# Kernel optimization log

Hardware: AMD Instinct MI355X
Metric: run time of the kernel (lower is better)

Reference implementation:

```python
import jax, jax.numpy as jnp
import numpy as np

D_MODEL = 512
HEAD = 64

def setup_inputs() -> dict:
    key = jax.random.key(0)
    ks = jax.random.split(key, 7)
    s_in = 1.0 / np.sqrt(D_MODEL)
    x = jax.random.normal(ks[0], (4, 4096, D_MODEL), dtype=jnp.float32)
    Wk = jax.random.uniform(ks[1], (D_MODEL, HEAD), jnp.float32, -s_in, s_in)
    bk = jax.random.uniform(ks[2], (HEAD,), jnp.float32, -s_in, s_in)
    Wq = jax.random.uniform(ks[3], (D_MODEL, HEAD), jnp.float32, -s_in, s_in)
    bq = jax.random.uniform(ks[4], (HEAD,), jnp.float32, -s_in, s_in)
    Wv = jax.random.uniform(ks[5], (D_MODEL, HEAD), jnp.float32, -s_in, s_in)
    bv = jax.random.uniform(ks[6], (HEAD,), jnp.float32, -s_in, s_in)
    return {"x": x, "Wk": Wk, "bk": bk, "Wq": Wq, "bq": bq, "Wv": Wv, "bv": bv}

def reference(x, Wk, bk, Wq, bq, Wv, bv):
    B, T, C = x.shape
    k = x @ Wk + bk            # [B,T,H]
    q = x @ Wq + bq            # [B,T,H]
    v = x @ Wv + bv            # [B,T,H]
    scale = C ** (-0.5)
    # NOTE: original computes k @ q^T (keys index rows), softmax over query axis
    w = jnp.einsum('bkh,bqh->bkq', k, q) * scale  # [B,T,T]
    w = jax.nn.softmax(w, axis=-1)
    out = jnp.einsum('bkq,bqh->bkh', w, v)        # [B,T,H]
    return out
```

## Files before the change

### kernel.cpp

```cpp
#include <hip/hip_runtime.h>


#define DM 512
#define HD 64
#define TSEQ 4096
#define KSCALE (1.4426950408889634f * 0.04419417382415922f)

typedef __attribute__((ext_vector_type(8))) __bf16 bf16x8;
typedef __attribute__((ext_vector_type(4))) __bf16 bf16x4;
typedef __attribute__((ext_vector_type(2))) __bf16 bf16x2;
typedef __attribute__((ext_vector_type(4))) float f32x4;
typedef __attribute__((ext_vector_type(16))) float f32x16;
typedef __attribute__((ext_vector_type(4))) unsigned int uint4v;

__device__ __forceinline__ float fast_exp2(float x) {
#if __has_builtin(__builtin_amdgcn_exp2f)
    return __builtin_amdgcn_exp2f(x);
#else
    return exp2f(x);
#endif
}

__device__ __forceinline__ bf16x8 ld_bf16x8(const unsigned short* p) {
    return __builtin_bit_cast(bf16x8, *(const uint4v*)p);
}
__device__ __forceinline__ f32x4 mfma16(bf16x8 a, bf16x8 b, f32x4 c) {
    return __builtin_amdgcn_mfma_f32_16x16x32_bf16(a, b, c, 0, 0, 0);
}
__device__ __forceinline__ f32x16 mfma32(bf16x8 a, bf16x8 b, f32x16 c) {
    return __builtin_amdgcn_mfma_f32_32x32x16_bf16(a, b, c, 0, 0, 0);
}

typedef const __attribute__((address_space(1))) unsigned int* gas_t;
typedef __attribute__((address_space(3))) unsigned int* las_t;
__device__ __forceinline__ void async_cp16(const void* g, void* l) {
    __builtin_amdgcn_global_load_lds((gas_t)(unsigned long long)g,
                                     (las_t)(unsigned int)(unsigned long long)l,
                                     16, 0, 0);
}

__global__ __launch_bounds__(256) void prep_wt(const float* __restrict__ Wk,
                                               const float* __restrict__ Wq,
                                               const float* __restrict__ Wv,
                                               unsigned short* __restrict__ WT) {
    int e = blockIdx.x * 256 + threadIdx.x;
    int m = e >> 15;
    int idx = e & 32767;
    int h = idx >> 9;
    int cc = idx & 511;
    const float* W = (m == 0) ? Wk : ((m == 1) ? Wq : Wv);
    float v = W[cc * HD + h];
    if (m == 0) v *= KSCALE;
    ((__bf16*)WT)[m * 32768 + h * DM + cc] = (__bf16)v;
}

__global__ __launch_bounds__(512, 4) void proj(const float* __restrict__ x,
                                               const unsigned short* __restrict__ WT,
                                               const float* __restrict__ bk,
                                               const float* __restrict__ bq,
                                               const float* __restrict__ bv,
                                               unsigned short* __restrict__ Kw,
                                               unsigned short* __restrict__ Qw,
                                               unsigned short* __restrict__ VTw) {
    __shared__ alignas(16) float xs[16384];
    const int tid = threadIdx.x;
    const int wv = tid >> 6, lane = tid & 63;
    const int c = lane & 15, quad = lane >> 4;
    const int ng = wv & 3, rg = wv >> 2;
    const int bx = blockIdx.x;
    const int n0 = ng * 16;

#pragma unroll
    for (int r = 0; r < 8; ++r) {
        int cid = r * 512 + tid;
        int row = cid >> 7, pos = cid & 127;
        int g = (pos & ~7) | ((pos ^ row) & 7);
        async_cp16((const char*)x + (size_t)(bx * 32 + row) * 2048 + g * 16,
                   (char*)xs + r * 8192 + wv * 1024);
    }
    __builtin_amdgcn_s_waitcnt(0x0f70);
    __syncthreads();

    const int arow = rg * 16 + c;
    const unsigned short* wtb = WT + (n0 + c) * DM + quad * 8;
    f32x4 acc[3];
#pragma unroll
    for (int m = 0; m < 3; ++m) acc[m] = (f32x4){0.f, 0.f, 0.f, 0.f};

#pragma unroll
    for (int ks = 0; ks < 16; ++ks) {
        int p0 = ks * 8 + quad * 2;
        int sp0 = (p0 & ~7) | ((p0 ^ arow) & 7);
        int sp1 = ((p0 + 1) & ~7) | (((p0 + 1) ^ arow) & 7);
        f32x4 xa = *(const f32x4*)((const char*)xs + arow * 2048 + sp0 * 16);
        f32x4 xb = *(const f32x4*)((const char*)xs + arow * 2048 + sp1 * 16);
        bf16x8 af;
        af[0] = (__bf16)xa[0]; af[1] = (__bf16)xa[1]; af[2] = (__bf16)xa[2]; af[3] = (__bf16)xa[3];
        af[4] = (__bf16)xb[0]; af[5] = (__bf16)xb[1]; af[6] = (__bf16)xb[2]; af[7] = (__bf16)xb[3];
#pragma unroll
        for (int m = 0; m < 3; ++m) {
            bf16x8 bf = ld_bf16x8(wtb + m * 32768 + ks * 32);
            acc[m] = mfma16(af, bf, acc[m]);
        }
    }

    const int row0 = bx * 32 + rg * 16 + quad * 4;
#pragma unroll
    for (int m = 0; m < 3; ++m) {
        const float* bp = (m == 0) ? bk : ((m == 1) ? bq : bv);
        float bias = bp[n0 + c];
        if (m == 0) bias *= KSCALE;
        if (m < 2) {
            __bf16* dst = (__bf16*)((m == 0) ? Kw : Qw);
#pragma unroll
            for (int r = 0; r < 4; ++r)
                dst[(row0 + r) * HD + n0 + c] = (__bf16)(acc[m][r] + bias);
        } else {
            bf16x4 pk;
#pragma unroll
            for (int r = 0; r < 4; ++r) pk[r] = (__bf16)(acc[m][r] + bias);
            int b = bx >> 7;
            int pj = bx & 127;
            int jsub = rg * 16 + quad * 4;
            *(bf16x4*)(VTw + (((size_t)(b * 128 + pj)) * 64 + n0 + c) * 32 + jsub) = pk;
        }
    }
}

__global__ __launch_bounds__(512, 2) void attn(const unsigned short* __restrict__ Kw,
                                               const unsigned short* __restrict__ Qw,
                                               const unsigned short* __restrict__ VTw,
                                               float* __restrict__ Op,
                                               float* __restrict__ Lp) {
    __shared__ alignas(16) char smem[131072];

    const int tid = threadIdx.x;
    const int wv = tid >> 6, lane = tid & 63;
    const int l5 = lane >> 5, l31 = lane & 31;
    const int rg = wv >> 2, jc = wv & 3;
    const int bx = blockIdx.x;
    const int batch = bx >> 6, js = (bx >> 5) & 1, tile = bx & 31;
    const int rowbase = batch * TSEQ + tile * 128;

    bf16x8 kf[2][4];
#pragma unroll
    for (int it = 0; it < 2; ++it) {
        const unsigned short* kp = Kw + (size_t)(rowbase + rg * 64 + it * 32 + l31) * HD;
#pragma unroll
        for (int ks = 0; ks < 4; ++ks) kf[it][ks] = ld_bf16x8(kp + ks * 16 + l5 * 8);
    }

    int qoff[4];
#pragma unroll
    for (int ks = 0; ks < 4; ++ks)
        qoff[ks] = l31 * 128 + (((ks * 2 + l5) ^ (l31 & 7)) * 16);
    int voff[2][2];
#pragma unroll
    for (int ht = 0; ht < 2; ++ht)
#pragma unroll
        for (int k2 = 0; k2 < 2; ++k2)
            voff[ht][k2] = (ht * 32 + l31) * 64 + (((k2 * 2 + l5) ^ (l31 & 3)) * 16);

    int qgo[4], vgo[4];
#pragma unroll
    for (int r = 0; r < 4; ++r) {
        qgo[r] = (r * 8 + (lane >> 3)) * 128 + (((lane & 7) ^ (lane >> 3)) * 16);
        vgo[r] = (r * 16 + (lane >> 2)) * 64 + (((lane & 3) ^ ((lane >> 2) & 3)) * 16);
    }
    const char* qg = (const char*)Qw + ((size_t)(batch * TSEQ + js * 2048 + jc * 32)) * 128;
    const char* vg = (const char*)VTw + ((size_t)(batch * 128 + js * 64 + jc)) * 4096;
    char* wbase = smem + wv * 16384;

    f32x16 o00, o01, o10, o11;
#pragma unroll
    for (int r = 0; r < 16; ++r) { o00[r] = 0.f; o01[r] = 0.f; o10[r] = 0.f; o11[r] = 0.f; }
    float lac0 = 0.f, lac1 = 0.f;

#pragma unroll
    for (int r = 0; r < 4; ++r) async_cp16(qg + qgo[r], wbase + r * 1024);
#pragma unroll
    for (int r = 0; r < 4; ++r) async_cp16(vg + vgo[r], wbase + 4096 + r * 1024);

    for (int jt = 0; jt < 16; ++jt) {
        if (jt < 15) {
            char* nb = wbase + ((jt + 1) & 1) * 8192;
            const char* qn = qg + (size_t)(jt + 1) * 16384;
            const char* vn = vg + (size_t)(jt + 1) * 16384;
#pragma unroll
            for (int r = 0; r < 4; ++r) async_cp16(qn + qgo[r], nb + r * 1024);
#pragma unroll
            for (int r = 0; r < 4; ++r) async_cp16(vn + vgo[r], nb + 4096 + r * 1024);
            __builtin_amdgcn_s_waitcnt(0x0f78);
        } else {
            __builtin_amdgcn_s_waitcnt(0x0f70);
        }
        const char* cb = wbase + (jt & 1) * 8192;
        const unsigned short* QL = (const unsigned short*)cb;
        const unsigned short* VL = (const unsigned short*)(cb + 4096);

        f32x16 s0, s1;
#pragma unroll
        for (int r = 0; r < 16; ++r) { s0[r] = 0.f; s1[r] = 0.f; }
#pragma unroll
        for (int ks = 0; ks < 4; ++ks) {
            bf16x8 qa = ld_bf16x8((const unsigned short*)((const char*)QL + qoff[ks]));
            s0 = mfma32(qa, kf[0][ks], s0);
            s1 = mfma32(qa, kf[1][ks], s1);
        }

        unsigned int pk0[8], pk1[8];
#pragma unroll
        for (int m = 0; m < 8; ++m) {
            float a0 = fast_exp2(s0[2 * m]), a1 = fast_exp2(s0[2 * m + 1]);
            float b0 = fast_exp2(s1[2 * m]), b1 = fast_exp2(s1[2 * m + 1]);
            lac0 += a0 + a1;
            lac1 += b0 + b1;
            bf16x2 ta; ta[0] = (__bf16)a0; ta[1] = (__bf16)a1;
            bf16x2 tb; tb[0] = (__bf16)b0; tb[1] = (__bf16)b1;
            pk0[m] = __builtin_bit_cast(unsigned int, ta);
            pk1[m] = __builtin_bit_cast(unsigned int, tb);
        }

#pragma unroll
        for (int k2 = 0; k2 < 2; ++k2) {
            bf16x8 pb0, pb1;
            {
                unsigned int A0 = pk0[k2 * 4 + 0], A1 = pk0[k2 * 4 + 1];
                unsigned int B0 = pk0[k2 * 4 + 2], B1 = pk0[k2 * 4 + 3];
                unsigned int t0 = l5 ? A0 : B0, t1 = l5 ? A1 : B1;
                unsigned int r0 = (unsigned int)__shfl_xor((int)t0, 32, 64);
                unsigned int r1 = (unsigned int)__shfl_xor((int)t1, 32, 64);
                uint4v u;
                u[0] = l5 ? r0 : A0; u[1] = l5 ? r1 : A1;
                u[2] = l5 ? B0 : r0; u[3] = l5 ? B1 : r1;
                pb0 = __builtin_bit_cast(bf16x8, u);
            }
            {
                unsigned int A0 = pk1[k2 * 4 + 0], A1 = pk1[k2 * 4 + 1];
                unsigned int B0 = pk1[k2 * 4 + 2], B1 = pk1[k2 * 4 + 3];
                unsigned int t0 = l5 ? A0 : B0, t1 = l5 ? A1 : B1;
                unsigned int r0 = (unsigned int)__shfl_xor((int)t0, 32, 64);
                unsigned int r1 = (unsigned int)__shfl_xor((int)t1, 32, 64);
                uint4v u;
                u[0] = l5 ? r0 : A0; u[1] = l5 ? r1 : A1;
                u[2] = l5 ? B0 : r0; u[3] = l5 ? B1 : r1;
                pb1 = __builtin_bit_cast(bf16x8, u);
            }
            bf16x8 vf0 = ld_bf16x8((const unsigned short*)((const char*)VL + voff[0][k2]));
            bf16x8 vf1 = ld_bf16x8((const unsigned short*)((const char*)VL + voff[1][k2]));
            o00 = mfma32(vf0, pb0, o00);
            o01 = mfma32(vf0, pb1, o01);
            o10 = mfma32(vf1, pb0, o10);
            o11 = mfma32(vf1, pb1, o11);
        }
    }

    lac0 += __shfl_xor(lac0, 32, 64);
    lac1 += __shfl_xor(lac1, 32, 64);
    __syncthreads();
    float* OCp = (float*)smem;
    float* ldsl = (float*)(smem + 34816);
    if (l5 == 0) {
        ldsl[jc * 128 + rg * 64 + l31] = lac0;
        ldsl[jc * 128 + rg * 64 + 32 + l31] = lac1;
    }

#pragma unroll
    for (int ph = 0; ph < 4; ++ph) {
        const int ht = ph >> 1, ih = ph & 1;
        __syncthreads();
        if (rg == ih) {
            const f32x16 oa = ht ? o10 : o00;
            const f32x16 ob = ht ? o11 : o01;
#pragma unroll
            for (int r = 0; r < 16; ++r) {
                int hr = (r & 3) + 8 * (r >> 2) + 4 * l5;
                OCp[(jc * 32 + hr) * 68 + l31] = oa[r];
                OCp[(jc * 32 + hr) * 68 + 32 + l31] = ob[r];
            }
        }
        __syncthreads();
#pragma unroll
        for (int rep = 0; rep < 4; ++rep) {
            int idx = rep * 512 + tid;
            int i = idx >> 5, hr = idx & 31;
            float v = OCp[(0 * 32 + hr) * 68 + i] + OCp[(1 * 32 + hr) * 68 + i]
                    + OCp[(2 * 32 + hr) * 68 + i] + OCp[(3 * 32 + hr) * 68 + i];
            Op[(size_t)js * 1048576 + (size_t)(rowbase + ih * 64 + i) * HD + ht * 32 + hr] = v;
        }
        if (ph == 0 && tid < 128) {
            float L = ldsl[tid] + ldsl[128 + tid] + ldsl[256 + tid] + ldsl[384 + tid];
            Lp[js * 16384 + rowbase + tid] = L;
        }
    }
}

__global__ __launch_bounds__(512) void fin(const float* __restrict__ Op,
                                           const float* __restrict__ Lp,
                                           float* __restrict__ out) {
    int idx = blockIdx.x * 512 + threadIdx.x;
    int e = idx * 4;
    int row = e >> 6;
    f32x4 a = *(const f32x4*)(Op + e);
    f32x4 b = *(const f32x4*)(Op + 1048576 + e);
    float L = Lp[row] + Lp[16384 + row];
    f32x4 r;
#pragma unroll
    for (int k = 0; k < 4; ++k) r[k] = (a[k] + b[k]) / L;
    *(f32x4*)(out + e) = r;
}

extern "C" void kernel_launch(void* const* d_in, const int* in_sizes, int n_in,
                              void* d_out, int out_size, void* d_ws, size_t ws_size,
                              hipStream_t stream) {
    (void)in_sizes; (void)n_in; (void)out_size; (void)ws_size;
    const float* x  = (const float*)d_in[0];
    const float* Wk = (const float*)d_in[1];
    const float* bk = (const float*)d_in[2];
    const float* Wq = (const float*)d_in[3];
    const float* bq = (const float*)d_in[4];
    const float* Wv = (const float*)d_in[5];
    const float* bv = (const float*)d_in[6];

    char* ws = (char*)d_ws;
    unsigned short* WT  = (unsigned short*)(ws);
    unsigned short* Kw  = (unsigned short*)(ws + 196608);
    unsigned short* Qw  = (unsigned short*)(ws + 2293760);
    unsigned short* VTw = (unsigned short*)(ws + 4390912);
    float* Opart        = (float*)(ws + 6488064);
    float* Lpart        = (float*)(ws + 14876672);
    float* outp = (float*)d_out;

    hipLaunchKernelGGL(prep_wt, dim3(384), dim3(256), 0, stream, Wk, Wq, Wv, WT);
    hipLaunchKernelGGL(proj, dim3(512), dim3(512), 0, stream,
                       x, WT, bk, bq, bv, Kw, Qw, VTw);
    hipLaunchKernelGGL(attn, dim3(256), dim3(512), 0, stream, Kw, Qw, VTw, Opart, Lpart);
    hipLaunchKernelGGL(fin, dim3(512), dim3(512), 0, stream, Opart, Lpart, outp);
}
```

Before: 138.9 us.

## Fuse all four stages into one cooperative kernel with grid syncs

```diff
diff --git a/kernel.cpp b/kernel.cpp
--- a/kernel.cpp
+++ b/kernel.cpp
@@ -1,10 +1,13 @@
 #include <hip/hip_runtime.h>
+#include <hip/hip_cooperative_groups.h>
 
 
 #define DM 512
 #define HD 64
 #define TSEQ 4096
 #define KSCALE (1.4426950408889634f * 0.04419417382415922f)
+
+namespace cg = cooperative_groups;
 
 typedef __attribute__((ext_vector_type(8))) __bf16 bf16x8;
 typedef __attribute__((ext_vector_type(4))) __bf16 bf16x4;
@@ -39,275 +42,290 @@
                                      16, 0, 0);
 }
 
-__global__ __launch_bounds__(256) void prep_wt(const float* __restrict__ Wk,
-                                               const float* __restrict__ Wq,
-                                               const float* __restrict__ Wv,
-                                               unsigned short* __restrict__ WT) {
-    int e = blockIdx.x * 256 + threadIdx.x;
-    int m = e >> 15;
-    int idx = e & 32767;
-    int h = idx >> 9;
-    int cc = idx & 511;
-    const float* W = (m == 0) ? Wk : ((m == 1) ? Wq : Wv);
-    float v = W[cc * HD + h];
-    if (m == 0) v *= KSCALE;
-    ((__bf16*)WT)[m * 32768 + h * DM + cc] = (__bf16)v;
-}
-
-__global__ __launch_bounds__(512, 4) void proj(const float* __restrict__ x,
-                                               const unsigned short* __restrict__ WT,
-                                               const float* __restrict__ bk,
-                                               const float* __restrict__ bq,
-                                               const float* __restrict__ bv,
-                                               unsigned short* __restrict__ Kw,
-                                               unsigned short* __restrict__ Qw,
-                                               unsigned short* __restrict__ VTw) {
-    __shared__ alignas(16) float xs[16384];
+__global__ __launch_bounds__(512) void mega(const float* __restrict__ x,
+                                            const float* __restrict__ Wk,
+                                            const float* __restrict__ bk,
+                                            const float* __restrict__ Wq,
+                                            const float* __restrict__ bq,
+                                            const float* __restrict__ Wv,
+                                            const float* __restrict__ bv,
+                                            unsigned short* __restrict__ WT,
+                                            unsigned short* __restrict__ Kw,
+                                            unsigned short* __restrict__ Qw,
+                                            unsigned short* __restrict__ VTw,
+                                            float* __restrict__ Op,
+                                            float* __restrict__ Lp,
+                                            float* __restrict__ out) {
+    __shared__ alignas(16) char smem[131072];
+    cg::grid_group grid = cg::this_grid();
+
     const int tid = threadIdx.x;
-    const int wv = tid >> 6, lane = tid & 63;
-    const int c = lane & 15, quad = lane >> 4;
-    const int ng = wv & 3, rg = wv >> 2;
-    const int bx = blockIdx.x;
-    const int n0 = ng * 16;
-
-#pragma unroll
-    for (int r = 0; r < 8; ++r) {
-        int cid = r * 512 + tid;
-        int row = cid >> 7, pos = cid & 127;
-        int g = (pos & ~7) | ((pos ^ row) & 7);
-        async_cp16((const char*)x + (size_t)(bx * 32 + row) * 2048 + g * 16,
-                   (char*)xs + r * 8192 + wv * 1024);
+    const int bxk = blockIdx.x;
+
+    if (tid < 384) {
+        int e = bxk * 384 + tid;
+        int m = e >> 15;
+        int idx = e & 32767;
+        int h = idx >> 9;
+        int cc = idx & 511;
+        const float* W = (m == 0) ? Wk : ((m == 1) ? Wq : Wv);
+        float v = W[cc * HD + h];
+        if (m == 0) v *= KSCALE;
+        ((__bf16*)WT)[m * 32768 + h * DM + cc] = (__bf16)v;
     }
-    __builtin_amdgcn_s_waitcnt(0x0f70);
-    __syncthreads();
-
-    const int arow = rg * 16 + c;
-    const unsigned short* wtb = WT + (n0 + c) * DM + quad * 8;
-    f32x4 acc[3];
-#pragma unroll
-    for (int m = 0; m < 3; ++m) acc[m] = (f32x4){0.f, 0.f, 0.f, 0.f};
-
-#pragma unroll
-    for (int ks = 0; ks < 16; ++ks) {
-        int p0 = ks * 8 + quad * 2;
-        int sp0 = (p0 & ~7) | ((p0 ^ arow) & 7);
-        int sp1 = ((p0 + 1) & ~7) | (((p0 + 1) ^ arow) & 7);
-        f32x4 xa = *(const f32x4*)((const char*)xs + arow * 2048 + sp0 * 16);
-        f32x4 xb = *(const f32x4*)((const char*)xs + arow * 2048 + sp1 * 16);
-        bf16x8 af;
-        af[0] = (__bf16)xa[0]; af[1] = (__bf16)xa[1]; af[2] = (__bf16)xa[2]; af[3] = (__bf16)xa[3];
-        af[4] = (__bf16)xb[0]; af[5] = (__bf16)xb[1]; af[6] = (__bf16)xb[2]; af[7] = (__bf16)xb[3];
-#pragma unroll
-        for (int m = 0; m < 3; ++m) {
-            bf16x8 bf = ld_bf16x8(wtb + m * 32768 + ks * 32);
-            acc[m] = mfma16(af, bf, acc[m]);
+    grid.sync();
+
+    {
+        const int wv = tid >> 6, lane = tid & 63;
+        const int c = lane & 15, quad = lane >> 4;
+        const int ng = wv & 3, rg = wv >> 2;
+        const int n0 = ng * 16;
+        const int arow = rg * 16 + c;
+
+#pragma unroll
+        for (int t = 0; t < 2; ++t) {
+            int bx = bxk * 2 + t;
+            float* xs = (float*)(smem + t * 65536);
+#pragma unroll
+            for (int r = 0; r < 8; ++r) {
+                int cid = r * 512 + tid;
+                int row = cid >> 7, pos = cid & 127;
+                int g = (pos & ~7) | ((pos ^ row) & 7);
+                async_cp16((const char*)x + (size_t)(bx * 32 + row) * 2048 + g * 16,
+                           (char*)xs + r * 8192 + wv * 1024);
+            }
+        }
+
+#pragma unroll
+        for (int t = 0; t < 2; ++t) {
+            int bx = bxk * 2 + t;
+            const float* xs = (const float*)(smem + t * 65536);
+            if (t == 0) __builtin_amdgcn_s_waitcnt(0x0f78);
+            else        __builtin_amdgcn_s_waitcnt(0x0f70);
+            __syncthreads();
+
+            const unsigned short* wtb = WT + (n0 + c) * DM + quad * 8;
+            f32x4 acc[3];
+#pragma unroll
+            for (int m = 0; m < 3; ++m) acc[m] = (f32x4){0.f, 0.f, 0.f, 0.f};
+
+#pragma unroll
+            for (int ks = 0; ks < 16; ++ks) {
+                int p0 = ks * 8 + quad * 2;
+                int sp0 = (p0 & ~7) | ((p0 ^ arow) & 7);
+                int sp1 = ((p0 + 1) & ~7) | (((p0 + 1) ^ arow) & 7);
+                f32x4 xa = *(const f32x4*)((const char*)xs + arow * 2048 + sp0 * 16);
+                f32x4 xb = *(const f32x4*)((const char*)xs + arow * 2048 + sp1 * 16);
+                bf16x8 af;
+                af[0] = (__bf16)xa[0]; af[1] = (__bf16)xa[1]; af[2] = (__bf16)xa[2]; af[3] = (__bf16)xa[3];
+                af[4] = (__bf16)xb[0]; af[5] = (__bf16)xb[1]; af[6] = (__bf16)xb[2]; af[7] = (__bf16)xb[3];
+#pragma unroll
+                for (int m = 0; m < 3; ++m) {
+                    bf16x8 bf = ld_bf16x8(wtb + m * 32768 + ks * 32);
+                    acc[m] = mfma16(af, bf, acc[m]);
+                }
+            }
+
+            const int row0 = bx * 32 + rg * 16 + quad * 4;
+#pragma unroll
+            for (int m = 0; m < 3; ++m) {
+                const float* bp = (m == 0) ? bk : ((m == 1) ? bq : bv);
+                float bias = bp[n0 + c];
+                if (m == 0) bias *= KSCALE;
+                if (m < 2) {
+                    __bf16* dst = (__bf16*)((m == 0) ? Kw : Qw);
+#pragma unroll
+                    for (int r = 0; r < 4; ++r)
+                        dst[(row0 + r) * HD + n0 + c] = (__bf16)(acc[m][r] + bias);
+                } else {
+                    bf16x4 pk;
+#pragma unroll
+                    for (int r = 0; r < 4; ++r) pk[r] = (__bf16)(acc[m][r] + bias);
+                    int b = bx >> 7;
+                    int pj = bx & 127;
+                    int jsub = rg * 16 + quad * 4;
+                    *(bf16x4*)(VTw + (((size_t)(b * 128 + pj)) * 64 + n0 + c) * 32 + jsub) = pk;
+                }
+            }
         }
     }
-
-    const int row0 = bx * 32 + rg * 16 + quad * 4;
-#pragma unroll
-    for (int m = 0; m < 3; ++m) {
-        const float* bp = (m == 0) ? bk : ((m == 1) ? bq : bv);
-        float bias = bp[n0 + c];
-        if (m == 0) bias *= KSCALE;
-        if (m < 2) {
-            __bf16* dst = (__bf16*)((m == 0) ? Kw : Qw);
-#pragma unroll
-            for (int r = 0; r < 4; ++r)
-                dst[(row0 + r) * HD + n0 + c] = (__bf16)(acc[m][r] + bias);
-        } else {
-            bf16x4 pk;
-#pragma unroll
-            for (int r = 0; r < 4; ++r) pk[r] = (__bf16)(acc[m][r] + bias);
-            int b = bx >> 7;
-            int pj = bx & 127;
-            int jsub = rg * 16 + quad * 4;
-            *(bf16x4*)(VTw + (((size_t)(b * 128 + pj)) * 64 + n0 + c) * 32 + jsub) = pk;
+    grid.sync();
+
+    {
+        const int wv = tid >> 6, lane = tid & 63;
+        const int l5 = lane >> 5, l31 = lane & 31;
+        const int rg = wv >> 2, jc = wv & 3;
+        const int bx = bxk;
+        const int batch = bx >> 6, js = (bx >> 5) & 1, tile = bx & 31;
+        const int rowbase = batch * TSEQ + tile * 128;
+
+        bf16x8 kf[2][4];
+#pragma unroll
+        for (int it = 0; it < 2; ++it) {
+            const unsigned short* kp = Kw + (size_t)(rowbase + rg * 64 + it * 32 + l31) * HD;
+#pragma unroll
+            for (int ks = 0; ks < 4; ++ks) kf[it][ks] = ld_bf16x8(kp + ks * 16 + l5 * 8);
+        }
+
+        int qoff[4];
+#pragma unroll
+        for (int ks = 0; ks < 4; ++ks)
+            qoff[ks] = l31 * 128 + (((ks * 2 + l5) ^ (l31 & 7)) * 16);
+        int voff[2][2];
+#pragma unroll
+        for (int ht = 0; ht < 2; ++ht)
+#pragma unroll
+            for (int k2 = 0; k2 < 2; ++k2)
+                voff[ht][k2] = (ht * 32 + l31) * 64 + (((k2 * 2 + l5) ^ (l31 & 3)) * 16);
+
+        int qgo[4], vgo[4];
+#pragma unroll
+        for (int r = 0; r < 4; ++r) {
+            qgo[r] = (r * 8 + (lane >> 3)) * 128 + (((lane & 7) ^ (lane >> 3)) * 16);
+            vgo[r] = (r * 16 + (lane >> 2)) * 64 + (((lane & 3) ^ ((lane >> 2) & 3)) * 16);
+        }
+        const char* qg = (const char*)Qw + ((size_t)(batch * TSEQ + js * 2048 + jc * 32)) * 128;
+        const char* vg = (const char*)VTw + ((size_t)(batch * 128 + js * 64 + jc)) * 4096;
+        char* wbase = smem + wv * 16384;
+
+        f32x16 o00, o01, o10, o11;
+#pragma unroll
+        for (int r = 0; r < 16; ++r) { o00[r] = 0.f; o01[r] = 0.f; o10[r] = 0.f; o11[r] = 0.f; }
+        float lac0 = 0.f, lac1 = 0.f;
+
+#pragma unroll
+        for (int r = 0; r < 4; ++r) async_cp16(qg + qgo[r], wbase + r * 1024);
+#pragma unroll
+        for (int r = 0; r < 4; ++r) async_cp16(vg + vgo[r], wbase + 4096 + r * 1024);
+
+        for (int jt = 0; jt < 16; ++jt) {
+            if (jt < 15) {
+                char* nb = wbase + ((jt + 1) & 1) * 8192;
+                const char* qn = qg + (size_t)(jt + 1) * 16384;
+                const char* vn = vg + (size_t)(jt + 1) * 16384;
+#pragma unroll
+                for (int r = 0; r < 4; ++r) async_cp16(qn + qgo[r], nb + r * 1024);
+#pragma unroll
+                for (int r = 0; r < 4; ++r) async_cp16(vn + vgo[r], nb + 4096 + r * 1024);
+                __builtin_amdgcn_s_waitcnt(0x0f78);
+            } else {
+                __builtin_amdgcn_s_waitcnt(0x0f70);
+            }
+            const char* cb = wbase + (jt & 1) * 8192;
+            const unsigned short* QL = (const unsigned short*)cb;
+            const unsigned short* VL = (const unsigned short*)(cb + 4096);
+
+            f32x16 s0, s1;
+#pragma unroll
+            for (int r = 0; r < 16; ++r) { s0[r] = 0.f; s1[r] = 0.f; }
+#pragma unroll
+            for (int ks = 0; ks < 4; ++ks) {
+                bf16x8 qa = ld_bf16x8((const unsigned short*)((const char*)QL + qoff[ks]));
+                s0 = mfma32(qa, kf[0][ks], s0);
+                s1 = mfma32(qa, kf[1][ks], s1);
+            }
+
+            unsigned int pk0[8], pk1[8];
+#pragma unroll
+            for (int m = 0; m < 8; ++m) {
+                float a0 = fast_exp2(s0[2 * m]), a1 = fast_exp2(s0[2 * m + 1]);
+                float b0 = fast_exp2(s1[2 * m]), b1 = fast_exp2(s1[2 * m + 1]);
+                lac0 += a0 + a1;
+                lac1 += b0 + b1;
+                bf16x2 ta; ta[0] = (__bf16)a0; ta[1] = (__bf16)a1;
+                bf16x2 tb; tb[0] = (__bf16)b0; tb[1] = (__bf16)b1;
+                pk0[m] = __builtin_bit_cast(unsigned int, ta);
+                pk1[m] = __builtin_bit_cast(unsigned int, tb);
+            }
+
+#pragma unroll
+            for (int k2 = 0; k2 < 2; ++k2) {
+                bf16x8 pb0, pb1;
+                {
+                    unsigned int A0 = pk0[k2 * 4 + 0], A1 = pk0[k2 * 4 + 1];
+                    unsigned int B0 = pk0[k2 * 4 + 2], B1 = pk0[k2 * 4 + 3];
+                    unsigned int t0 = l5 ? A0 : B0, t1 = l5 ? A1 : B1;
+                    unsigned int r0 = (unsigned int)__shfl_xor((int)t0, 32, 64);
+                    unsigned int r1 = (unsigned int)__shfl_xor((int)t1, 32, 64);
+                    uint4v u;
+                    u[0] = l5 ? r0 : A0; u[1] = l5 ? r1 : A1;
+                    u[2] = l5 ? B0 : r0; u[3] = l5 ? B1 : r1;
+                    pb0 = __builtin_bit_cast(bf16x8, u);
+                }
+                {
+                    unsigned int A0 = pk1[k2 * 4 + 0], A1 = pk1[k2 * 4 + 1];
+                    unsigned int B0 = pk1[k2 * 4 + 2], B1 = pk1[k2 * 4 + 3];
+                    unsigned int t0 = l5 ? A0 : B0, t1 = l5 ? A1 : B1;
+                    unsigned int r0 = (unsigned int)__shfl_xor((int)t0, 32, 64);
+                    unsigned int r1 = (unsigned int)__shfl_xor((int)t1, 32, 64);
+                    uint4v u;
+                    u[0] = l5 ? r0 : A0; u[1] = l5 ? r1 : A1;
+                    u[2] = l5 ? B0 : r0; u[3] = l5 ? B1 : r1;
+                    pb1 = __builtin_bit_cast(bf16x8, u);
+                }
+                bf16x8 vf0 = ld_bf16x8((const unsigned short*)((const char*)VL + voff[0][k2]));
+                bf16x8 vf1 = ld_bf16x8((const unsigned short*)((const char*)VL + voff[1][k2]));
+                o00 = mfma32(vf0, pb0, o00);
+                o01 = mfma32(vf0, pb1, o01);
+                o10 = mfma32(vf1, pb0, o10);
+                o11 = mfma32(vf1, pb1, o11);
+            }
+        }
+
+        lac0 += __shfl_xor(lac0, 32, 64);
+        lac1 += __shfl_xor(lac1, 32, 64);
+        __syncthreads();
+        float* OCp = (float*)smem;
+        float* ldsl = (float*)(smem + 34816);
+        if (l5 == 0) {
+            ldsl[jc * 128 + rg * 64 + l31] = lac0;
+            ldsl[jc * 128 + rg * 64 + 32 + l31] = lac1;
+        }
+
+#pragma unroll
+        for (int ph = 0; ph < 4; ++ph) {
+            const int ht = ph >> 1, ih = ph & 1;
+            __syncthreads();
+            if (rg == ih) {
+                const f32x16 oa = ht ? o10 : o00;
+                const f32x16 ob = ht ? o11 : o01;
+#pragma unroll
+                for (int r = 0; r < 16; ++r) {
+                    int hr = (r & 3) + 8 * (r >> 2) + 4 * l5;
+                    OCp[(jc * 32 + hr) * 68 + l31] = oa[r];
+                    OCp[(jc * 32 + hr) * 68 + 32 + l31] = ob[r];
+                }
+            }
+            __syncthreads();
+#pragma unroll
+            for (int rep = 0; rep < 4; ++rep) {
+                int idx = rep * 512 + tid;
+                int i = idx >> 5, hr = idx & 31;
+                float v = OCp[(0 * 32 + hr) * 68 + i] + OCp[(1 * 32 + hr) * 68 + i]
+                        + OCp[(2 * 32 + hr) * 68 + i] + OCp[(3 * 32 + hr) * 68 + i];
+                Op[(size_t)js * 1048576 + (size_t)(rowbase + ih * 64 + i) * HD + ht * 32 + hr] = v;
+            }
+            if (ph == 0 && tid < 128) {
+                float L = ldsl[tid] + ldsl[128 + tid] + ldsl[256 + tid] + ldsl[384 + tid];
+                Lp[js * 16384 + rowbase + tid] = L;
+            }
         }
     }
-}
-
-__global__ __launch_bounds__(512, 2) void attn(const unsigned short* __restrict__ Kw,
-                                               const unsigned short* __restrict__ Qw,
-                                               const unsigned short* __restrict__ VTw,
-                                               float* __restrict__ Op,
-                                               float* __restrict__ Lp) {
-    __shared__ alignas(16) char smem[131072];
-
-    const int tid = threadIdx.x;
-    const int wv = tid >> 6, lane = tid & 63;
-    const int l5 = lane >> 5, l31 = lane & 31;
-    const int rg = wv >> 2, jc = wv & 3;
-    const int bx = blockIdx.x;
-    const int batch = bx >> 6, js = (bx >> 5) & 1, tile = bx & 31;
-    const int rowbase = batch * TSEQ + tile * 128;
-
-    bf16x8 kf[2][4];
-#pragma unroll
-    for (int it = 0; it < 2; ++it) {
-        const unsigned short* kp = Kw + (size_t)(rowbase + rg * 64 + it * 32 + l31) * HD;
-#pragma unroll
-        for (int ks = 0; ks < 4; ++ks) kf[it][ks] = ld_bf16x8(kp + ks * 16 + l5 * 8);
+    grid.sync();
+
+#pragma unroll
+    for (int t = 0; t < 2; ++t) {
+        int idx = bxk * 1024 + t * 512 + tid;
+        int e = idx * 4;
+        int row = e >> 6;
+        f32x4 a = *(const f32x4*)(Op + e);
+        f32x4 b = *(const f32x4*)(Op + 1048576 + e);
+        float L = Lp[row] + Lp[16384 + row];
+        f32x4 r;
+#pragma unroll
+        for (int k = 0; k < 4; ++k) r[k] = (a[k] + b[k]) / L;
+        *(f32x4*)(out + e) = r;
     }
-
-    int qoff[4];
-#pragma unroll
-    for (int ks = 0; ks < 4; ++ks)
-        qoff[ks] = l31 * 128 + (((ks * 2 + l5) ^ (l31 & 7)) * 16);
-    int voff[2][2];
-#pragma unroll
-    for (int ht = 0; ht < 2; ++ht)
-#pragma unroll
-        for (int k2 = 0; k2 < 2; ++k2)
-            voff[ht][k2] = (ht * 32 + l31) * 64 + (((k2 * 2 + l5) ^ (l31 & 3)) * 16);
-
-    int qgo[4], vgo[4];
-#pragma unroll
-    for (int r = 0; r < 4; ++r) {
-        qgo[r] = (r * 8 + (lane >> 3)) * 128 + (((lane & 7) ^ (lane >> 3)) * 16);
-        vgo[r] = (r * 16 + (lane >> 2)) * 64 + (((lane & 3) ^ ((lane >> 2) & 3)) * 16);
-    }
-    const char* qg = (const char*)Qw + ((size_t)(batch * TSEQ + js * 2048 + jc * 32)) * 128;
-    const char* vg = (const char*)VTw + ((size_t)(batch * 128 + js * 64 + jc)) * 4096;
-    char* wbase = smem + wv * 16384;
-
-    f32x16 o00, o01, o10, o11;
-#pragma unroll
-    for (int r = 0; r < 16; ++r) { o00[r] = 0.f; o01[r] = 0.f; o10[r] = 0.f; o11[r] = 0.f; }
-    float lac0 = 0.f, lac1 = 0.f;
-
-#pragma unroll
-    for (int r = 0; r < 4; ++r) async_cp16(qg + qgo[r], wbase + r * 1024);
-#pragma unroll
-    for (int r = 0; r < 4; ++r) async_cp16(vg + vgo[r], wbase + 4096 + r * 1024);
-
-    for (int jt = 0; jt < 16; ++jt) {
-        if (jt < 15) {
-            char* nb = wbase + ((jt + 1) & 1) * 8192;
-            const char* qn = qg + (size_t)(jt + 1) * 16384;
-            const char* vn = vg + (size_t)(jt + 1) * 16384;
-#pragma unroll
-            for (int r = 0; r < 4; ++r) async_cp16(qn + qgo[r], nb + r * 1024);
-#pragma unroll
-            for (int r = 0; r < 4; ++r) async_cp16(vn + vgo[r], nb + 4096 + r * 1024);
-            __builtin_amdgcn_s_waitcnt(0x0f78);
-        } else {
-            __builtin_amdgcn_s_waitcnt(0x0f70);
-        }
-        const char* cb = wbase + (jt & 1) * 8192;
-        const unsigned short* QL = (const unsigned short*)cb;
-        const unsigned short* VL = (const unsigned short*)(cb + 4096);
-
-        f32x16 s0, s1;
-#pragma unroll
-        for (int r = 0; r < 16; ++r) { s0[r] = 0.f; s1[r] = 0.f; }
-#pragma unroll
-        for (int ks = 0; ks < 4; ++ks) {
-            bf16x8 qa = ld_bf16x8((const unsigned short*)((const char*)QL + qoff[ks]));
-            s0 = mfma32(qa, kf[0][ks], s0);
-            s1 = mfma32(qa, kf[1][ks], s1);
-        }
-
-        unsigned int pk0[8], pk1[8];
-#pragma unroll
-        for (int m = 0; m < 8; ++m) {
-            float a0 = fast_exp2(s0[2 * m]), a1 = fast_exp2(s0[2 * m + 1]);
-            float b0 = fast_exp2(s1[2 * m]), b1 = fast_exp2(s1[2 * m + 1]);
-            lac0 += a0 + a1;
-            lac1 += b0 + b1;
-            bf16x2 ta; ta[0] = (__bf16)a0; ta[1] = (__bf16)a1;
-            bf16x2 tb; tb[0] = (__bf16)b0; tb[1] = (__bf16)b1;
-            pk0[m] = __builtin_bit_cast(unsigned int, ta);
-            pk1[m] = __builtin_bit_cast(unsigned int, tb);
-        }
-
-#pragma unroll
-        for (int k2 = 0; k2 < 2; ++k2) {
-            bf16x8 pb0, pb1;
-            {
-                unsigned int A0 = pk0[k2 * 4 + 0], A1 = pk0[k2 * 4 + 1];
-                unsigned int B0 = pk0[k2 * 4 + 2], B1 = pk0[k2 * 4 + 3];
-                unsigned int t0 = l5 ? A0 : B0, t1 = l5 ? A1 : B1;
-                unsigned int r0 = (unsigned int)__shfl_xor((int)t0, 32, 64);
-                unsigned int r1 = (unsigned int)__shfl_xor((int)t1, 32, 64);
-                uint4v u;
-                u[0] = l5 ? r0 : A0; u[1] = l5 ? r1 : A1;
-                u[2] = l5 ? B0 : r0; u[3] = l5 ? B1 : r1;
-                pb0 = __builtin_bit_cast(bf16x8, u);
-            }
-            {
-                unsigned int A0 = pk1[k2 * 4 + 0], A1 = pk1[k2 * 4 + 1];
-                unsigned int B0 = pk1[k2 * 4 + 2], B1 = pk1[k2 * 4 + 3];
-                unsigned int t0 = l5 ? A0 : B0, t1 = l5 ? A1 : B1;
-                unsigned int r0 = (unsigned int)__shfl_xor((int)t0, 32, 64);
-                unsigned int r1 = (unsigned int)__shfl_xor((int)t1, 32, 64);
-                uint4v u;
-                u[0] = l5 ? r0 : A0; u[1] = l5 ? r1 : A1;
-                u[2] = l5 ? B0 : r0; u[3] = l5 ? B1 : r1;
-                pb1 = __builtin_bit_cast(bf16x8, u);
-            }
-            bf16x8 vf0 = ld_bf16x8((const unsigned short*)((const char*)VL + voff[0][k2]));
-            bf16x8 vf1 = ld_bf16x8((const unsigned short*)((const char*)VL + voff[1][k2]));
-            o00 = mfma32(vf0, pb0, o00);
-            o01 = mfma32(vf0, pb1, o01);
-            o10 = mfma32(vf1, pb0, o10);
-            o11 = mfma32(vf1, pb1, o11);
-        }
-    }
-
-    lac0 += __shfl_xor(lac0, 32, 64);
-    lac1 += __shfl_xor(lac1, 32, 64);
-    __syncthreads();
-    float* OCp = (float*)smem;
-    float* ldsl = (float*)(smem + 34816);
-    if (l5 == 0) {
-        ldsl[jc * 128 + rg * 64 + l31] = lac0;
-        ldsl[jc * 128 + rg * 64 + 32 + l31] = lac1;
-    }
-
-#pragma unroll
-    for (int ph = 0; ph < 4; ++ph) {
-        const int ht = ph >> 1, ih = ph & 1;
-        __syncthreads();
-        if (rg == ih) {
-            const f32x16 oa = ht ? o10 : o00;
-            const f32x16 ob = ht ? o11 : o01;
-#pragma unroll
-            for (int r = 0; r < 16; ++r) {
-                int hr = (r & 3) + 8 * (r >> 2) + 4 * l5;
-                OCp[(jc * 32 + hr) * 68 + l31] = oa[r];
-                OCp[(jc * 32 + hr) * 68 + 32 + l31] = ob[r];
-            }
-        }
-        __syncthreads();
-#pragma unroll
-        for (int rep = 0; rep < 4; ++rep) {
-            int idx = rep * 512 + tid;
-            int i = idx >> 5, hr = idx & 31;
-            float v = OCp[(0 * 32 + hr) * 68 + i] + OCp[(1 * 32 + hr) * 68 + i]
-                    + OCp[(2 * 32 + hr) * 68 + i] + OCp[(3 * 32 + hr) * 68 + i];
-            Op[(size_t)js * 1048576 + (size_t)(rowbase + ih * 64 + i) * HD + ht * 32 + hr] = v;
-        }
-        if (ph == 0 && tid < 128) {
-            float L = ldsl[tid] + ldsl[128 + tid] + ldsl[256 + tid] + ldsl[384 + tid];
-            Lp[js * 16384 + rowbase + tid] = L;
-        }
-    }
-}
-
-__global__ __launch_bounds__(512) void fin(const float* __restrict__ Op,
-                                           const float* __restrict__ Lp,
-                                           float* __restrict__ out) {
-    int idx = blockIdx.x * 512 + threadIdx.x;
-    int e = idx * 4;
-    int row = e >> 6;
-    f32x4 a = *(const f32x4*)(Op + e);
-    f32x4 b = *(const f32x4*)(Op + 1048576 + e);
-    float L = Lp[row] + Lp[16384 + row];
-    f32x4 r;
-#pragma unroll
-    for (int k = 0; k < 4; ++k) r[k] = (a[k] + b[k]) / L;
-    *(f32x4*)(out + e) = r;
 }
 
 extern "C" void kernel_launch(void* const* d_in, const int* in_sizes, int n_in,
@@ -331,9 +349,8 @@
     float* Lpart        = (float*)(ws + 14876672);
     float* outp = (float*)d_out;
 
-    hipLaunchKernelGGL(prep_wt, dim3(384), dim3(256), 0, stream, Wk, Wq, Wv, WT);
-    hipLaunchKernelGGL(proj, dim3(512), dim3(512), 0, stream,
-                       x, WT, bk, bq, bv, Kw, Qw, VTw);
-    hipLaunchKernelGGL(attn, dim3(256), dim3(512), 0, stream, Kw, Qw, VTw, Opart, Lpart);
-    hipLaunchKernelGGL(fin, dim3(512), dim3(512), 0, stream, Opart, Lpart, outp);
-}
+    void* args[] = {(void*)&x, (void*)&Wk, (void*)&bk, (void*)&Wq, (void*)&bq,
+                    (void*)&Wv, (void*)&bv, (void*)&WT, (void*)&Kw, (void*)&Qw,
+                    (void*)&VTw, (void*)&Opart, (void*)&Lpart, (void*)&outp};
+    hipLaunchCooperativeKernel((void*)mega, dim3(256), dim3(512), args, 0, stream);
+}
```

Measured after the change: 234.6 us. 68.9% more time.

## Load attention Q/V fragments directly into registers and halve proj tile size

Applied to the files above, without the earlier changes.

```diff
diff --git a/kernel.cpp b/kernel.cpp
--- a/kernel.cpp
+++ b/kernel.cpp
@@ -54,7 +54,7 @@
     ((__bf16*)WT)[m * 32768 + h * DM + cc] = (__bf16)v;
 }
 
-__global__ __launch_bounds__(512, 4) void proj(const float* __restrict__ x,
+__global__ __launch_bounds__(256, 4) void proj(const float* __restrict__ x,
                                                const unsigned short* __restrict__ WT,
                                                const float* __restrict__ bk,
                                                const float* __restrict__ bq,
@@ -62,26 +62,24 @@
                                                unsigned short* __restrict__ Kw,
                                                unsigned short* __restrict__ Qw,
                                                unsigned short* __restrict__ VTw) {
-    __shared__ alignas(16) float xs[16384];
+    __shared__ alignas(16) float xs[8192];
     const int tid = threadIdx.x;
     const int wv = tid >> 6, lane = tid & 63;
     const int c = lane & 15, quad = lane >> 4;
-    const int ng = wv & 3, rg = wv >> 2;
     const int bx = blockIdx.x;
-    const int n0 = ng * 16;
+    const int n0 = wv * 16;
 
 #pragma unroll
     for (int r = 0; r < 8; ++r) {
-        int cid = r * 512 + tid;
+        int cid = r * 256 + tid;
         int row = cid >> 7, pos = cid & 127;
         int g = (pos & ~7) | ((pos ^ row) & 7);
-        async_cp16((const char*)x + (size_t)(bx * 32 + row) * 2048 + g * 16,
-                   (char*)xs + r * 8192 + wv * 1024);
+        async_cp16((const char*)x + (size_t)(bx * 16 + row) * 2048 + g * 16,
+                   (char*)xs + r * 4096 + wv * 1024);
     }
     __builtin_amdgcn_s_waitcnt(0x0f70);
     __syncthreads();
 
-    const int arow = rg * 16 + c;
     const unsigned short* wtb = WT + (n0 + c) * DM + quad * 8;
     f32x4 acc[3];
 #pragma unroll
@@ -90,10 +88,10 @@
 #pragma unroll
     for (int ks = 0; ks < 16; ++ks) {
         int p0 = ks * 8 + quad * 2;
-        int sp0 = (p0 & ~7) | ((p0 ^ arow) & 7);
-        int sp1 = ((p0 + 1) & ~7) | (((p0 + 1) ^ arow) & 7);
-        f32x4 xa = *(const f32x4*)((const char*)xs + arow * 2048 + sp0 * 16);
-        f32x4 xb = *(const f32x4*)((const char*)xs + arow * 2048 + sp1 * 16);
+        int sp0 = (p0 & ~7) | ((p0 ^ c) & 7);
+        int sp1 = ((p0 + 1) & ~7) | (((p0 + 1) ^ c) & 7);
+        f32x4 xa = *(const f32x4*)((const char*)xs + c * 2048 + sp0 * 16);
+        f32x4 xb = *(const f32x4*)((const char*)xs + c * 2048 + sp1 * 16);
         bf16x8 af;
         af[0] = (__bf16)xa[0]; af[1] = (__bf16)xa[1]; af[2] = (__bf16)xa[2]; af[3] = (__bf16)xa[3];
         af[4] = (__bf16)xb[0]; af[5] = (__bf16)xb[1]; af[6] = (__bf16)xb[2]; af[7] = (__bf16)xb[3];
@@ -104,7 +102,7 @@
         }
     }
 
-    const int row0 = bx * 32 + rg * 16 + quad * 4;
+    const int row0 = bx * 16 + quad * 4;
 #pragma unroll
     for (int m = 0; m < 3; ++m) {
         const float* bp = (m == 0) ? bk : ((m == 1) ? bq : bv);
@@ -119,9 +117,10 @@
             bf16x4 pk;
 #pragma unroll
             for (int r = 0; r < 4; ++r) pk[r] = (__bf16)(acc[m][r] + bias);
-            int b = bx >> 7;
-            int pj = bx & 127;
-            int jsub = rg * 16 + quad * 4;
+            int b = bx >> 8;
+            int t16 = bx & 255;
+            int pj = t16 >> 1;
+            int jsub = (t16 & 1) * 16 + quad * 4;
             *(bf16x4*)(VTw + (((size_t)(b * 128 + pj)) * 64 + n0 + c) * 32 + jsub) = pk;
         }
     }
@@ -132,7 +131,7 @@
                                                const unsigned short* __restrict__ VTw,
                                                float* __restrict__ Op,
                                                float* __restrict__ Lp) {
-    __shared__ alignas(16) char smem[131072];
+    __shared__ alignas(16) char smem[36864];
 
     const int tid = threadIdx.x;
     const int wv = tid >> 6, lane = tid & 63;
@@ -150,62 +149,48 @@
         for (int ks = 0; ks < 4; ++ks) kf[it][ks] = ld_bf16x8(kp + ks * 16 + l5 * 8);
     }
 
-    int qoff[4];
-#pragma unroll
-    for (int ks = 0; ks < 4; ++ks)
-        qoff[ks] = l31 * 128 + (((ks * 2 + l5) ^ (l31 & 7)) * 16);
-    int voff[2][2];
-#pragma unroll
-    for (int ht = 0; ht < 2; ++ht)
-#pragma unroll
-        for (int k2 = 0; k2 < 2; ++k2)
-            voff[ht][k2] = (ht * 32 + l31) * 64 + (((k2 * 2 + l5) ^ (l31 & 3)) * 16);
-
-    int qgo[4], vgo[4];
-#pragma unroll
-    for (int r = 0; r < 4; ++r) {
-        qgo[r] = (r * 8 + (lane >> 3)) * 128 + (((lane & 7) ^ (lane >> 3)) * 16);
-        vgo[r] = (r * 16 + (lane >> 2)) * 64 + (((lane & 3) ^ ((lane >> 2) & 3)) * 16);
-    }
-    const char* qg = (const char*)Qw + ((size_t)(batch * TSEQ + js * 2048 + jc * 32)) * 128;
-    const char* vg = (const char*)VTw + ((size_t)(batch * 128 + js * 64 + jc)) * 4096;
-    char* wbase = smem + wv * 16384;
+    const char* qg = (const char*)Qw
+                   + ((size_t)(batch * TSEQ + js * 2048 + jc * 32 + l31)) * 128
+                   + l5 * 16;
+    const char* vg = (const char*)VTw
+                   + ((size_t)(batch * 128 + js * 64 + jc)) * 4096
+                   + l31 * 64 + l5 * 16;
 
     f32x16 o00, o01, o10, o11;
 #pragma unroll
     for (int r = 0; r < 16; ++r) { o00[r] = 0.f; o01[r] = 0.f; o10[r] = 0.f; o11[r] = 0.f; }
     float lac0 = 0.f, lac1 = 0.f;
 
-#pragma unroll
-    for (int r = 0; r < 4; ++r) async_cp16(qg + qgo[r], wbase + r * 1024);
-#pragma unroll
-    for (int r = 0; r < 4; ++r) async_cp16(vg + vgo[r], wbase + 4096 + r * 1024);
+    bf16x8 qa[4], vf[2][2];
+#pragma unroll
+    for (int ks = 0; ks < 4; ++ks) qa[ks] = ld_bf16x8((const unsigned short*)(qg + ks * 32));
+#pragma unroll
+    for (int ht = 0; ht < 2; ++ht)
+#pragma unroll
+        for (int k2 = 0; k2 < 2; ++k2)
+            vf[ht][k2] = ld_bf16x8((const unsigned short*)(vg + ht * 2048 + k2 * 32));
 
     for (int jt = 0; jt < 16; ++jt) {
+        bf16x8 qn[4], vn[2][2];
         if (jt < 15) {
-            char* nb = wbase + ((jt + 1) & 1) * 8192;
-            const char* qn = qg + (size_t)(jt + 1) * 16384;
-            const char* vn = vg + (size_t)(jt + 1) * 16384;
-#pragma unroll
-            for (int r = 0; r < 4; ++r) async_cp16(qn + qgo[r], nb + r * 1024);
-#pragma unroll
-            for (int r = 0; r < 4; ++r) async_cp16(vn + vgo[r], nb + 4096 + r * 1024);
-            __builtin_amdgcn_s_waitcnt(0x0f78);
-        } else {
-            __builtin_amdgcn_s_waitcnt(0x0f70);
-        }
-        const char* cb = wbase + (jt & 1) * 8192;
-        const unsigned short* QL = (const unsigned short*)cb;
-        const unsigned short* VL = (const unsigned short*)(cb + 4096);
+            const char* q1 = qg + (size_t)(jt + 1) * 16384;
+            const char* v1 = vg + (size_t)(jt + 1) * 16384;
+#pragma unroll
+            for (int ks = 0; ks < 4; ++ks) qn[ks] = ld_bf16x8((const unsigned short*)(q1 + ks * 32));
+#pragma unroll
+            for (int ht = 0; ht < 2; ++ht)
+#pragma unroll
+                for (int k2 = 0; k2 < 2; ++k2)
+                    vn[ht][k2] = ld_bf16x8((const unsigned short*)(v1 + ht * 2048 + k2 * 32));
+        }
 
         f32x16 s0, s1;
 #pragma unroll
         for (int r = 0; r < 16; ++r) { s0[r] = 0.f; s1[r] = 0.f; }
 #pragma unroll
         for (int ks = 0; ks < 4; ++ks) {
-            bf16x8 qa = ld_bf16x8((const unsigned short*)((const char*)QL + qoff[ks]));
-            s0 = mfma32(qa, kf[0][ks], s0);
-            s1 = mfma32(qa, kf[1][ks], s1);
+            s0 = mfma32(qa[ks], kf[0][ks], s0);
+            s1 = mfma32(qa[ks], kf[1][ks], s1);
         }
 
         unsigned int pk0[8], pk1[8];
@@ -246,13 +231,18 @@
                 u[2] = l5 ? B0 : r0; u[3] = l5 ? B1 : r1;
                 pb1 = __builtin_bit_cast(bf16x8, u);
             }
-            bf16x8 vf0 = ld_bf16x8((const unsigned short*)((const char*)VL + voff[0][k2]));
-            bf16x8 vf1 = ld_bf16x8((const unsigned short*)((const char*)VL + voff[1][k2]));
-            o00 = mfma32(vf0, pb0, o00);
-            o01 = mfma32(vf0, pb1, o01);
-            o10 = mfma32(vf1, pb0, o10);
-            o11 = mfma32(vf1, pb1, o11);
-        }
+            o00 = mfma32(vf[0][k2], pb0, o00);
+            o01 = mfma32(vf[0][k2], pb1, o01);
+            o10 = mfma32(vf[1][k2], pb0, o10);
+            o11 = mfma32(vf[1][k2], pb1, o11);
+        }
+
+#pragma unroll
+        for (int ks = 0; ks < 4; ++ks) qa[ks] = qn[ks];
+#pragma unroll
+        for (int ht = 0; ht < 2; ++ht)
+#pragma unroll
+            for (int k2 = 0; k2 < 2; ++k2) vf[ht][k2] = vn[ht][k2];
     }
 
     lac0 += __shfl_xor(lac0, 32, 64);
@@ -332,7 +322,7 @@
     float* outp = (float*)d_out;
 
     hipLaunchKernelGGL(prep_wt, dim3(384), dim3(256), 0, stream, Wk, Wq, Wv, WT);
-    hipLaunchKernelGGL(proj, dim3(512), dim3(512), 0, stream,
+    hipLaunchKernelGGL(proj, dim3(1024), dim3(256), 0, stream,
                        x, WT, bk, bq, bv, Kw, Qw, VTw);
     hipLaunchKernelGGL(attn, dim3(256), dim3(512), 0, stream, Kw, Qw, VTw, Opart, Lpart);
     hipLaunchKernelGGL(fin, dim3(512), dim3(512), 0, stream, Opart, Lpart, outp);
```

After: 141.3 us. Within noise of the previous version (+1.7%).
